# Kernel tuning notes

Measured on AMD Instinct MI355X. Metric: run time of the kernel, lower is better.

The kernel has to match this reference:

```python
import jax, jax.numpy as jnp
import numpy as np

B, C, L = 16, 64, 512
L_P = 16
D_MODEL = 1024
STRIDE = 8
N_P = (L - L_P) // STRIDE + 2  # 64 patches
PERIOD = L // 2                # statsmodels period = series_input_length / 2


def setup_inputs() -> dict:
    key = jax.random.key(0)
    ks = jax.random.split(key, 11)
    s = 0.02  # small init scale for weights
    return {
        "data_x": jax.random.normal(ks[0], (B, C, L), jnp.float32),
        "gamma": jax.random.uniform(ks[1], (B, C, L), jnp.float32),
        "beta": jax.random.uniform(ks[2], (B, C, L), jnp.float32),
        "w_trend": jax.random.normal(ks[3], (L_P, L), jnp.float32) * s,
        "b_trend": jax.random.normal(ks[4], (L_P,), jnp.float32) * s,
        "w_seasonal": jax.random.normal(ks[5], (L_P, L), jnp.float32) * s,
        "b_seasonal": jax.random.normal(ks[6], (L_P,), jnp.float32) * s,
        "w_resid": jax.random.normal(ks[7], (L_P, L), jnp.float32) * s,
        "b_resid": jax.random.normal(ks[8], (L_P,), jnp.float32) * s,
        "w_g": jax.random.normal(ks[9], (D_MODEL, 3 * L_P), jnp.float32) * s,
        "b_g": jax.random.normal(ks[10], (D_MODEL,), jnp.float32) * s,
    }


def _decompose(x):
    """Vectorized statsmodels seasonal_decompose(model='additive', period=L//2).

    trend: centered moving average with filter [0.5,1,...,1,0.5]/p (even period),
           NaN edges -> replaced by 0 (as in the torch module).
    seasonal: per-phase nanmean of detrended, demeaned, tiled to length L.
    resid: detrended - seasonal on the valid (non-NaN) region, 0 elsewhere.
    x: [B, C, L] -> (trend, seasonal, resid) each [B, C, L].
    """
    p = PERIOD
    filt = jnp.concatenate([jnp.full((1,), 0.5, x.dtype),
                            jnp.ones((p - 1,), x.dtype),
                            jnp.full((1,), 0.5, x.dtype)]) / p  # len p+1 (p even)
    head = p // 2               # leading NaN count (filter is symmetric)
    nvalid = L - p              # valid trend samples
    xf = x.reshape(B * C, 1, L)
    tv = jax.lax.conv_general_dilated(xf, filt.reshape(1, 1, p + 1),
                                      (1,), "VALID")[:, 0, :]  # [BC, L-p]
    trend = jnp.zeros((B * C, L), x.dtype).at[:, head:head + nvalid].set(tv)
    dv = x.reshape(B * C, L)[:, head:head + nvalid] - tv  # detrended, valid region
    # per-phase nanmean over valid detrended samples
    phase = (head + jnp.arange(nvalid)) % p               # phase of each valid index
    sums = jnp.zeros((B * C, p), x.dtype).at[:, phase].add(dv)
    counts = jnp.zeros((p,), x.dtype).at[phase].add(1.0)
    pa = sums / counts                                    # period averages [BC, p]
    pa = pa - jnp.mean(pa, axis=1, keepdims=True)
    seasonal = jnp.tile(pa, (1, L // p))                  # L = 2p exactly
    resid = jnp.zeros((B * C, L), x.dtype).at[:, head:head + nvalid].set(
        dv - seasonal[:, head:head + nvalid])
    return (trend.reshape(B, C, L), seasonal.reshape(B, C, L),
            resid.reshape(B, C, L))


def reference(data_x, gamma, beta, w_trend, b_trend, w_seasonal, b_seasonal,
              w_resid, b_resid, w_g, b_g):
    # 'transformed': per-channel stats (dim=1), torch var is unbiased (ddof=1), epsi=0
    mean = jnp.mean(data_x, axis=1)
    var = jnp.var(data_x, axis=1, ddof=1)
    mean = (mean / jnp.sqrt(var))[:, None, :]             # [B,1,L] broadcast over C
    x = gamma * (data_x - mean) + beta
    x = jax.lax.stop_gradient(x)                          # season() detaches
    trend, seasonal, resid = _decompose(x)
    t = trend @ w_trend.T + b_trend                       # [B,C,L_p]
    s = seasonal @ w_seasonal.T + b_seasonal
    r = resid @ w_resid.T + b_resid
    feats = jnp.concatenate([t, s, r], axis=-1)           # [B,C,3*L_p]
    feats = jnp.broadcast_to(feats[:, :, None, :], (B, C, N_P, 3 * L_P))
    return feats @ w_g.T + b_g                            # [B,C,N_p,D_MODEL]
```

## Files before the change

### kernel.cpp

```cpp
#include <hip/hip_runtime.h>
#include <math.h>

#define BB   16
#define CC   64
#define LL   512
#define LP   16
#define DM   1024
#define NP   64
#define PRD  256
#define HEAD 128
#define NV   256

typedef float f32x4 __attribute__((ext_vector_type(4)));

#define OFF_WGT 0

__global__ __launch_bounds__(256) void transpose_kernel(
    const float* __restrict__ w_g, float* __restrict__ ws)
{
    const int tid = threadIdx.x, bid = blockIdx.x;
    int base = bid * 3072 + tid;
#pragma unroll
    for (int k = 0; k < 12; ++k) {
        int e = base + k * 256;
        int j = e >> 10, d = e & 1023;
        ws[OFF_WGT + e] = w_g[d * 48 + j];
    }
}

__global__ __launch_bounds__(256) void fused_kernel(
    const float* __restrict__ dx,    const float* __restrict__ gamma,
    const float* __restrict__ beta,  const float* __restrict__ w_t,
    const float* __restrict__ b_t,   const float* __restrict__ w_s,
    const float* __restrict__ b_s,   const float* __restrict__ w_r,
    const float* __restrict__ b_r,   const float* __restrict__ b_g,
    const float* __restrict__ ws,    float* __restrict__ out)
{
    __shared__ __align__(16) float xs[LL];
    __shared__ __align__(16) float pps[LL/2 + 1];
    __shared__ __align__(16) float tvs[NV];
    __shared__ __align__(16) float pas[PRD];
    __shared__ __align__(16) float feats[48];
    __shared__ float wsum[4];
    __shared__ float wred[4];

    const int tid  = threadIdx.x;
    const int lane = tid & 63;
    const int wv   = tid >> 6;
    const int bc   = blockIdx.x;
    const int b    = bc >> 6;
    const int cown = bc & 63;

    const float2* dxb = (const float2*)(dx + (size_t)b * CC * LL);
    float2 sv = make_float2(0.f, 0.f), qv = make_float2(0.f, 0.f);
    float2 xv = make_float2(0.f, 0.f);
#pragma unroll 8
    for (int c = 0; c < CC; ++c) {
        float2 v = dxb[c * 256 + tid];
        if (c == cown) xv = v;
        sv.x += v.x;       sv.y += v.y;
        qv.x += v.x * v.x; qv.y += v.y * v.y;
    }
    float2 mp;
    {
        float mx = sv.x * (1.0f / CC), my = sv.y * (1.0f / CC);
        float vx = (qv.x - (float)CC * mx * mx) * (1.0f / (CC - 1));
        float vy = (qv.y - (float)CC * my * my) * (1.0f / (CC - 1));
        mp.x = mx / sqrtf(vx);
        mp.y = my / sqrtf(vy);
    }

    const size_t base = (size_t)bc * LL;
    float2 gv = ((const float2*)(gamma + base))[tid];
    float2 bv = ((const float2*)(beta  + base))[tid];
    float2 xp;
    xp.x = gv.x * (xv.x - mp.x) + bv.x;
    xp.y = gv.y * (xv.y - mp.y) + bv.y;
    ((float2*)xs)[tid] = xp;

    float v = xp.x + xp.y;
#pragma unroll
    for (int d = 1; d < 64; d <<= 1) {
        float t = __shfl_up(v, d, 64);
        if (lane >= d) v += t;
    }
    if (lane == 63) wsum[wv] = v;
    __syncthreads();
    float off = 0.f;
    for (int w = 0; w < wv; ++w) off += wsum[w];
    pps[tid + 1] = v + off;
    if (tid == 0) pps[0] = 0.f;
    __syncthreads();

    const int i  = tid;
    const int k2 = i + 257;
    const float Pi = pps[i  >> 1] + ((i  & 1) ? xs[i  & ~1] : 0.f);
    const float Pk = pps[k2 >> 1] + ((k2 & 1) ? xs[k2 & ~1] : 0.f);
    const float tv = (Pk - Pi - 0.5f * (xs[i] + xs[i + 256])) * (1.0f / 256.0f);
    tvs[i] = tv;
    const float dv = xs[HEAD + i] - tv;

    float r = dv;
#pragma unroll
    for (int m = 32; m; m >>= 1) r += __shfl_xor(r, m, 64);
    if (lane == 0) wred[wv] = r;
    __syncthreads();
    const float mdv = (wred[0] + wred[1] + wred[2] + wred[3]) * (1.0f / 256.0f);

    pas[(i + 128) & 255] = dv - mdv;
    __syncthreads();

    {
        const int g  = tid >> 4;
        const int ln = tid & 15;
        const f32x4* wt4  = (const f32x4*)(w_t + g * LL + HEAD);
        const f32x4* ws4a = (const f32x4*)(w_s + g * LL);
        const f32x4* ws4b = (const f32x4*)(w_s + g * LL + PRD);
        const f32x4* wr4  = (const f32x4*)(w_r + g * LL + HEAD);
        const f32x4* tv4  = (const f32x4*)tvs;
        const f32x4* pa4  = (const f32x4*)pas;
        float at = 0.f, as = 0.f, ar = 0.f;
#pragma unroll
        for (int q = 0; q < 4; ++q) {
            const int m = ln * 4 + q;
            f32x4 t  = tv4[m],  p  = pa4[m];
            f32x4 a  = wt4[m];
            f32x4 s1 = ws4a[m], s2 = ws4b[m];
            f32x4 rr = wr4[m];
            at += t.x * a.x + t.y * a.y + t.z * a.z + t.w * a.w;
            as += p.x * (s1.x + s2.x) + p.y * (s1.y + s2.y)
                + p.z * (s1.z + s2.z) + p.w * (s1.w + s2.w);
            ar += rr.x + rr.y + rr.z + rr.w;
        }
#pragma unroll
        for (int msk = 8; msk; msk >>= 1) {
            at += __shfl_xor(at, msk, 64);
            as += __shfl_xor(as, msk, 64);
            ar += __shfl_xor(ar, msk, 64);
        }
        if (ln == 0) {
            feats[g]      = at + b_t[g];
            feats[16 + g] = as + b_s[g];
            feats[32 + g] = mdv * ar + b_r[g];
        }
    }
    __syncthreads();

    const f32x4* wT4 = (const f32x4*)(ws + OFF_WGT);
    f32x4 acc = ((const f32x4*)b_g)[tid];
#pragma unroll
    for (int j = 0; j < 48; ++j)
        acc += feats[j] * wT4[j * 256 + tid];

    f32x4* op = (f32x4*)out + (size_t)bc * (NP * DM / 4) + tid;
#pragma unroll
    for (int n = 0; n < NP; ++n)
        op[(size_t)n * (DM / 4)] = acc;
}

extern "C" void kernel_launch(void* const* d_in, const int* in_sizes, int n_in,
                              void* d_out, int out_size, void* d_ws, size_t ws_size,
                              hipStream_t stream) {
    const float* dx    = (const float*)d_in[0];
    const float* gamma = (const float*)d_in[1];
    const float* beta  = (const float*)d_in[2];
    const float* w_t   = (const float*)d_in[3];
    const float* b_t   = (const float*)d_in[4];
    const float* w_s   = (const float*)d_in[5];
    const float* b_s   = (const float*)d_in[6];
    const float* w_r   = (const float*)d_in[7];
    const float* b_r   = (const float*)d_in[8];
    const float* w_g   = (const float*)d_in[9];
    const float* b_g   = (const float*)d_in[10];
    float* out = (float*)d_out;
    float* ws  = (float*)d_ws;

    transpose_kernel<<<16, 256, 0, stream>>>(w_g, ws);
    fused_kernel<<<BB * CC, 256, 0, stream>>>(
        dx, gamma, beta, w_t, b_t, w_s, b_s, w_r, b_r, b_g, ws, out);
}
```

Measured before the change: 66.68 us.

## Drop w_g transpose kernel and read w_g rows directly with quad shuffle-reduce

Removes the separate transpose launch and computes the final projection by reading w_g in its native [D_MODEL,48] layout. Each group of four lanes covers one output row, reduces with xor shuffles, and stages the results in shared memory. The output write loop is restructured so each wave writes 16 patch rows with four contiguous float4 stores. This saves a kernel launch and the workspace round trip, but adds a shared-memory stage and an extra barrier per block.

New measurement: 65.26 us. -2.1%, faster.

```diff
diff --git a/kernel.cpp b/kernel.cpp
--- a/kernel.cpp
+++ b/kernel.cpp
@@ -13,34 +13,20 @@
 
 typedef float f32x4 __attribute__((ext_vector_type(4)));
 
-#define OFF_WGT 0
-
-__global__ __launch_bounds__(256) void transpose_kernel(
-    const float* __restrict__ w_g, float* __restrict__ ws)
-{
-    const int tid = threadIdx.x, bid = blockIdx.x;
-    int base = bid * 3072 + tid;
-#pragma unroll
-    for (int k = 0; k < 12; ++k) {
-        int e = base + k * 256;
-        int j = e >> 10, d = e & 1023;
-        ws[OFF_WGT + e] = w_g[d * 48 + j];
-    }
-}
-
 __global__ __launch_bounds__(256) void fused_kernel(
     const float* __restrict__ dx,    const float* __restrict__ gamma,
     const float* __restrict__ beta,  const float* __restrict__ w_t,
     const float* __restrict__ b_t,   const float* __restrict__ w_s,
     const float* __restrict__ b_s,   const float* __restrict__ w_r,
-    const float* __restrict__ b_r,   const float* __restrict__ b_g,
-    const float* __restrict__ ws,    float* __restrict__ out)
+    const float* __restrict__ b_r,   const float* __restrict__ w_g,
+    const float* __restrict__ b_g,   float* __restrict__ out)
 {
     __shared__ __align__(16) float xs[LL];
     __shared__ __align__(16) float pps[LL/2 + 1];
     __shared__ __align__(16) float tvs[NV];
     __shared__ __align__(16) float pas[PRD];
     __shared__ __align__(16) float feats[48];
+    __shared__ __align__(16) float sres[DM];
     __shared__ float wsum[4];
     __shared__ float wred[4];
 
@@ -146,16 +132,44 @@
     }
     __syncthreads();
 
-    const f32x4* wT4 = (const f32x4*)(ws + OFF_WGT);
-    f32x4 acc = ((const f32x4*)b_g)[tid];
+    {
+        const int qsl = lane & 3;
+        float fs[12];
 #pragma unroll
-    for (int j = 0; j < 48; ++j)
-        acc += feats[j] * wT4[j * 256 + tid];
+        for (int k = 0; k < 12; ++k) fs[k] = feats[qsl * 12 + k];
 
-    f32x4* op = (f32x4*)out + (size_t)bc * (NP * DM / 4) + tid;
+        const f32x4* wg4 = (const f32x4*)w_g;
+#pragma unroll 4
+        for (int p = 0; p < 16; ++p) {
+            const int drow = p * 64 + wv * 16 + (lane >> 2);
+            const int wbase = (p * 64 + wv * 16) * 12 + 3 * lane;
+            f32x4 w0 = wg4[wbase + 0];
+            f32x4 w1 = wg4[wbase + 1];
+            f32x4 w2 = wg4[wbase + 2];
+            float acc = fs[0]*w0.x + fs[1]*w0.y + fs[2]*w0.z + fs[3]*w0.w
+                      + fs[4]*w1.x + fs[5]*w1.y + fs[6]*w1.z + fs[7]*w1.w
+                      + fs[8]*w2.x + fs[9]*w2.y + fs[10]*w2.z + fs[11]*w2.w;
+            acc += __shfl_xor(acc, 1, 64);
+            acc += __shfl_xor(acc, 2, 64);
+            if (qsl == 0) sres[drow] = acc + b_g[drow];
+        }
+    }
+    __syncthreads();
+
+    const f32x4* s4 = (const f32x4*)sres;
+    const f32x4 v0 = s4[lane];
+    const f32x4 v1 = s4[64 + lane];
+    const f32x4 v2 = s4[128 + lane];
+    const f32x4 v3 = s4[192 + lane];
+    f32x4* op = (f32x4*)out + (size_t)bc * (NP * DM / 4)
+              + (size_t)(wv * 16) * (DM / 4) + lane;
 #pragma unroll
-    for (int n = 0; n < NP; ++n)
-        op[(size_t)n * (DM / 4)] = acc;
+    for (int n = 0; n < 16; ++n) {
+        op[n * (DM / 4) +   0] = v0;
+        op[n * (DM / 4) +  64] = v1;
+        op[n * (DM / 4) + 128] = v2;
+        op[n * (DM / 4) + 192] = v3;
+    }
 }
 
 extern "C" void kernel_launch(void* const* d_in, const int* in_sizes, int n_in,
@@ -173,9 +187,7 @@
     const float* w_g   = (const float*)d_in[9];
     const float* b_g   = (const float*)d_in[10];
     float* out = (float*)d_out;
-    float* ws  = (float*)d_ws;
 
-    transpose_kernel<<<16, 256, 0, stream>>>(w_g, ws);
     fused_kernel<<<BB * CC, 256, 0, stream>>>(
-        dx, gamma, beta, w_t, b_t, w_s, b_s, w_r, b_r, b_g, ws, out);
+        dx, gamma, beta, w_t, b_t, w_s, b_s, w_r, b_r, w_g, b_g, out);
 }
```
